# Optimization experiments

Hardware: AMD Instinct MI355X
Metric: run time of the kernel (lower is better)

The kernel has to match this reference:

```python
import jax, jax.numpy as jnp
import numpy as np

N = 50000      # nodes
E = 800000     # edges (before self-loops)
G = 128        # graphs in batch
IN = 128       # in_channels
HID = 32       # hidden_channels (per head)
HEADS = 4
OUT = 64       # out_channels
SLOPE = 0.2    # PyG GATConv default negative_slope


def setup_inputs() -> dict:
    key = jax.random.key(0)
    ks = jax.random.split(key, 24)
    s = 0.1
    inp = {
        'x': jax.random.normal(ks[0], (N, IN), jnp.float32),
        'edge_index': jax.random.randint(ks[1], (2, E), 0, N, dtype=jnp.int32),
        'batch': jnp.sort(jax.random.randint(ks[2], (N,), 0, G, dtype=jnp.int32)),
        # conv1: IN -> HEADS*HID, concat
        'W1': jax.random.normal(ks[3], (IN, HEADS * HID), jnp.float32) * s,
        'a1s': jax.random.normal(ks[4], (HEADS, HID), jnp.float32) * s,
        'a1d': jax.random.normal(ks[5], (HEADS, HID), jnp.float32) * s,
        'b1': jnp.zeros((HEADS * HID,), jnp.float32),
        # conv2: HEADS*HID -> HEADS*HID, concat
        'W2': jax.random.normal(ks[6], (HEADS * HID, HEADS * HID), jnp.float32) * s,
        'a2s': jax.random.normal(ks[7], (HEADS, HID), jnp.float32) * s,
        'a2d': jax.random.normal(ks[8], (HEADS, HID), jnp.float32) * s,
        'b2': jnp.zeros((HEADS * HID,), jnp.float32),
        # conv3
        'W3': jax.random.normal(ks[9], (HEADS * HID, HEADS * HID), jnp.float32) * s,
        'a3s': jax.random.normal(ks[10], (HEADS, HID), jnp.float32) * s,
        'a3d': jax.random.normal(ks[11], (HEADS, HID), jnp.float32) * s,
        'b3': jnp.zeros((HEADS * HID,), jnp.float32),
        # conv4: heads=1, concat=False -> HID
        'W4': jax.random.normal(ks[12], (HEADS * HID, 1 * HID), jnp.float32) * s,
        'a4s': jax.random.normal(ks[13], (1, HID), jnp.float32) * s,
        'a4d': jax.random.normal(ks[14], (1, HID), jnp.float32) * s,
        'b4': jnp.zeros((HID,), jnp.float32),
        # fc: HID -> OUT
        'fcW': jax.random.normal(ks[15], (HID, OUT), jnp.float32) * s,
        'fcb': jnp.zeros((OUT,), jnp.float32),
    }
    return inp


def gat_conv(x, src, dst, W, a_src, a_dst, bias, heads, ch, concat):
    # x: [N, F_in]; src/dst: [E'] with self-loops (PyG add_self_loops=True)
    h = (x @ W).reshape(N, heads, ch)                       # [N, H, C]
    alpha_s = jnp.einsum('nhc,hc->nh', h, a_src)            # [N, H]
    alpha_d = jnp.einsum('nhc,hc->nh', h, a_dst)
    e = jax.nn.leaky_relu(alpha_s[src] + alpha_d[dst], SLOPE)  # [E', H]
    # segment softmax over edges grouped by destination node
    e_max = jax.ops.segment_max(e, dst, num_segments=N)
    e = jnp.exp(e - e_max[dst])
    denom = jax.ops.segment_sum(e, dst, num_segments=N)
    alpha = e / (denom[dst] + 1e-16)                        # [E', H]
    msg = h[src] * alpha[:, :, None]                        # [E', H, C]
    out = jax.ops.segment_sum(msg, dst, num_segments=N)     # [N, H, C]
    out = out.reshape(N, heads * ch) if concat else out.mean(axis=1)
    return out + bias


def reference(x, edge_index, batch, W1, a1s, a1d, b1, W2, a2s, a2d, b2,
              W3, a3s, a3d, b3, W4, a4s, a4d, b4, fcW, fcb):
    loop = jnp.arange(N, dtype=edge_index.dtype)
    src = jnp.concatenate([edge_index[0], loop])            # add self-loops once
    dst = jnp.concatenate([edge_index[1], loop])
    h = jax.nn.elu(gat_conv(x, src, dst, W1, a1s, a1d, b1, HEADS, HID, True))
    h = jax.nn.elu(gat_conv(h, src, dst, W2, a2s, a2d, b2, HEADS, HID, True))
    h = jax.nn.elu(gat_conv(h, src, dst, W3, a3s, a3d, b3, HEADS, HID, True))
    h = jax.nn.elu(gat_conv(h, src, dst, W4, a4s, a4d, b4, 1, HID, False))
    # global mean pool over graphs
    counts = jax.ops.segment_sum(jnp.ones((N,), h.dtype), batch, num_segments=G)
    pooled = jax.ops.segment_sum(h, batch, num_segments=G) / jnp.maximum(counts, 1.0)[:, None]
    # dropout p=0.5 is identity at inference
    return pooled @ fcW + fcb                               # [G, OUT]
```

## Files before the change

kernel.cpp:

```cpp
#include <hip/hip_runtime.h>
#include <hip/hip_bf16.h>


constexpr int NN     = 50000;
constexpr int NNPAD  = 50048;
constexpr int EE     = 800000;
constexpr int ETOT   = EE + NN;
constexpr int GG     = 128;
constexpr int HIDC   = 32;
constexpr int OUTC   = 64;

constexpr int NRANGE = (NN + 127) / 128;
constexpr int EPB    = 4096;
constexpr int NBLK   = (EE + EPB - 1) / EPB;
constexpr int RCAP   = 2688;

typedef short  bf16x8 __attribute__((ext_vector_type(8)));
typedef float  f32x4  __attribute__((ext_vector_type(4)));

static __device__ __forceinline__ unsigned short f2bf(float f) {
    __hip_bfloat16 h = __float2bfloat16(f);
    unsigned short u; __builtin_memcpy(&u, &h, 2); return u;
}
static __device__ __forceinline__ unsigned int f2bf2(float lo, float hi) {
    __hip_bfloat162 h2 = __float22bfloat162_rn(make_float2(lo, hi));
    unsigned int u; __builtin_memcpy(&u, &h2, 4); return u;
}
static __device__ __forceinline__ float bflo(unsigned int v) {
    return __uint_as_float(v << 16);
}
static __device__ __forceinline__ float bfhi(unsigned int v) {
    return __uint_as_float(v & 0xffff0000u);
}
static __device__ __forceinline__ float elu(float v) {
    return (v > 0.f) ? v : (__expf(v) - 1.f);
}
static __device__ __forceinline__ float leaky(float e) {
    return fmaxf(e, 0.f) + 0.2f * fminf(e, 0.f);
}

static __device__ void local_sort_body(
    char* smem, const int* __restrict__ ei,
    unsigned int* __restrict__ blocksorted, int* __restrict__ boffs, int b)
{
    unsigned int* sorted = reinterpret_cast<unsigned int*>(smem);
    int* hist  = reinterpret_cast<int*>(smem + EPB * 4);
    int* scanv = hist + (NRANGE + 1);
    int* cur   = scanv + (NRANGE + 1);
    int* wsum4 = cur + (NRANGE + 1);
    int* ct_s  = wsum4 + 4;

    const int tid = threadIdx.x;
    const int lane = tid & 63, wid = tid >> 6;
    const int e0 = b * EPB;
    const int ecnt = min(EPB, EE - e0);

    for (int t = tid; t < NRANGE + 1; t += 256) hist[t] = 0;
    __syncthreads();

    unsigned int recs[16];
    int rkey[16];
#pragma unroll
    for (int k = 0; k < 16; ++k) {
        const int idx = tid + k * 256;
        rkey[k] = -1;
        if (idx < ecnt) {
            const int src = ei[e0 + idx];
            const int dst = ei[EE + e0 + idx];
            const int r = dst >> 7;
            recs[k] = (unsigned int)src | ((unsigned int)(dst & 127) << 16);
            rkey[k] = r;
            atomicAdd(&hist[r], 1);
        }
    }
    __syncthreads();

    int carry = 0;
    for (int base = 0; base < NRANGE + 1; base += 256) {
        const int i = base + tid;
        const int v = (i < NRANGE + 1) ? hist[i] : 0;
        int incl = v;
#pragma unroll
        for (int off = 1; off < 64; off <<= 1) {
            int t = __shfl_up(incl, off, 64);
            if (lane >= off) incl += t;
        }
        if (lane == 63) wsum4[wid] = incl;
        __syncthreads();
        if (tid == 0) {
            int s = 0;
#pragma unroll
            for (int w = 0; w < 4; ++w) { int t = wsum4[w]; wsum4[w] = s; s += t; }
            *ct_s = s;
        }
        __syncthreads();
        const int excl = carry + wsum4[wid] + incl - v;
        if (i < NRANGE + 1) { scanv[i] = excl; cur[i] = excl; }
        carry += *ct_s;
        __syncthreads();
    }

#pragma unroll
    for (int k = 0; k < 16; ++k) {
        if (rkey[k] >= 0) {
            const int pos = atomicAdd(&cur[rkey[k]], 1);
            sorted[pos] = recs[k];
        }
    }
    __syncthreads();

    for (int t = tid; t < ecnt; t += 256)
        blocksorted[(size_t)b * EPB + t] = sorted[t];
    for (int t = tid; t < NRANGE + 1; t += 256)
        boffs[b * (NRANGE + 1) + t] = scanv[t];
}

template<int F_OUT, int NH, bool XF32>
static __device__ void gemm_body(
    char* smem, const void* __restrict__ xv,
    const unsigned short* __restrict__ wtg,
    unsigned short* __restrict__ hb,
    float* __restrict__ as_out, float* __restrict__ ad_out, int bid)
{
    constexpr int F_STG = F_OUT + 16;
    unsigned short* wt = reinterpret_cast<unsigned short*>(smem);
    const int tid = threadIdx.x;

    {
        const bf16x8* __restrict__ wg = reinterpret_cast<const bf16x8*>(wtg);
        bf16x8* wl = reinterpret_cast<bf16x8*>(wt);
        constexpr int NV = F_STG * 16;
#pragma unroll
        for (int i = 0; i < NV / 256; ++i)
            wl[i * 256 + tid] = wg[i * 256 + tid];
    }
    __syncthreads();

    const int wave = tid >> 6, lane = tid & 63;
    const int kchunk = (lane >> 4) * 8;
    const int kb_base = (lane >> 4) * 16;

#pragma unroll
    for (int rr = 0; rr < 2; ++rr) {
        const int row0 = bid * 128 + rr * 64 + wave * 16;
        const int arow = row0 + (lane & 15);

        bf16x8 a[4];
        if (XF32) {
            if (arow < NN) {
                const float* __restrict__ ap = (const float*)xv + (size_t)arow * 128;
#pragma unroll
                for (int ks = 0; ks < 4; ++ks) {
                    const float4 f0 = *reinterpret_cast<const float4*>(ap + ks * 32 + kchunk);
                    const float4 f1 = *reinterpret_cast<const float4*>(ap + ks * 32 + kchunk + 4);
                    uint4 u;
                    u.x = f2bf2(f0.x, f0.y);
                    u.y = f2bf2(f0.z, f0.w);
                    u.z = f2bf2(f1.x, f1.y);
                    u.w = f2bf2(f1.z, f1.w);
                    bf16x8 v; __builtin_memcpy(&v, &u, 16);
                    a[ks] = v;
                }
            } else {
#pragma unroll
                for (int ks = 0; ks < 4; ++ks) a[ks] = bf16x8{0,0,0,0,0,0,0,0};
            }
        } else {
            const unsigned short* __restrict__ ap =
                (const unsigned short*)xv + (size_t)arow * 128;
#pragma unroll
            for (int ks = 0; ks < 4; ++ks)
                a[ks] = *reinterpret_cast<const bf16x8*>(ap + ks * 32 + kchunk);
        }

        const int rbase = row0 + (lane >> 4) * 4;

#pragma unroll
        for (int nt = 0; nt < F_OUT / 16; ++nt) {
            const int n = nt * 16 + (lane & 15);
            f32x4 acc = {0.f, 0.f, 0.f, 0.f};
#pragma unroll
            for (int ks = 0; ks < 4; ++ks) {
                const int byte = n * 256 + ((ks * 64 + kb_base) ^ ((n & 7) << 4));
                bf16x8 b = *reinterpret_cast<const bf16x8*>(
                    reinterpret_cast<const char*>(wt) + byte);
                acc = __builtin_amdgcn_mfma_f32_16x16x32_bf16(a[ks], b, acc, 0, 0, 0);
            }
#pragma unroll
            for (int r = 0; r < 4; ++r) {
                const int row = rbase + r;
                if (row < NN)
                    hb[(size_t)row * F_OUT + n] = f2bf(acc[r]);
            }
        }

        {
            const int n = F_OUT + (lane & 15);
            f32x4 acc = {0.f, 0.f, 0.f, 0.f};
#pragma unroll
            for (int ks = 0; ks < 4; ++ks) {
                const int byte = n * 256 + ((ks * 64 + kb_base) ^ ((n & 7) << 4));
                bf16x8 b = *reinterpret_cast<const bf16x8*>(
                    reinterpret_cast<const char*>(wt) + byte);
                acc = __builtin_amdgcn_mfma_f32_16x16x32_bf16(a[ks], b, acc, 0, 0, 0);
            }
            const int col = lane & 15;
            if (col < 8) {
                const int hh = col & 3;
                const bool is_d = col >= 4;
                if (hh < NH) {
                    float* op = is_d ? ad_out : as_out;
#pragma unroll
                    for (int r = 0; r < 4; ++r) {
                        const int row = rbase + r;
                        if (row < NN) {
                            if (NH == 4) op[row * 4 + hh] = acc[r];
                            else         op[row]          = acc[r];
                        }
                    }
                }
            }
        }
    }
}

constexpr int FUSED_SMEM = 144 * 128 * 2;

__global__ __launch_bounds__(256) void fused_ls_gemm1_kernel(
    const int* __restrict__ ei,
    unsigned int* __restrict__ blocksorted,
    int* __restrict__ boffs,
    const float* __restrict__ x,
    const unsigned short* __restrict__ wtg,
    unsigned short* __restrict__ hb,
    float* __restrict__ as_out, float* __restrict__ ad_out)
{
    __shared__ char smem[FUSED_SMEM];
    if (blockIdx.x < NBLK)
        local_sort_body(smem, ei, blocksorted, boffs, blockIdx.x);
    else
        gemm_body<128, 4, true>(smem, x, wtg, hb, as_out, ad_out,
                                blockIdx.x - NBLK);
}

template<int F_OUT, int NH>
__global__ __launch_bounds__(256) void gemm_mfma_kernel(
    const void* __restrict__ xv,
    const unsigned short* __restrict__ wtg,
    unsigned short* __restrict__ hb,
    float* __restrict__ as_out, float* __restrict__ ad_out)
{
    __shared__ char smem[(F_OUT + 16) * 128 * 2];
    gemm_body<F_OUT, NH, false>(smem, xv, wtg, hb, as_out, ad_out, blockIdx.x);
}

__global__ __launch_bounds__(256) void rtot_kernel(const int* __restrict__ boffs,
                                                   int* __restrict__ rtot)
{
    const int r = blockIdx.x * 4 + (threadIdx.x >> 6);
    const int lane = threadIdx.x & 63;
    if (r >= NRANGE) return;
    int tot = 0;
    for (int b = lane; b < NBLK; b += 64) {
        const int* bp = boffs + b * (NRANGE + 1) + r;
        tot += bp[1] - bp[0];
    }
#pragma unroll
    for (int k = 1; k < 64; k <<= 1) tot += __shfl_xor(tot, k, 64);
    if (lane == 0) rtot[r] = tot + min(128, NN - r * 128);
}

__global__ __launch_bounds__(512) void rscan_kernel(const int* __restrict__ rtot,
                                                    int* __restrict__ rbase)
{
    __shared__ int wsum[8], wpre[8];
    const int tid = threadIdx.x, lane = tid & 63, wid = tid >> 6;
    int tot = (tid < NRANGE) ? rtot[tid] : 0;
    int incl = tot;
#pragma unroll
    for (int off = 1; off < 64; off <<= 1) {
        int t = __shfl_up(incl, off, 64);
        if (lane >= off) incl += t;
    }
    if (lane == 63) wsum[wid] = incl;
    __syncthreads();
    if (tid < 8) {
        int wv = wsum[tid], winc = wv;
#pragma unroll
        for (int off = 1; off < 8; off <<= 1) {
            int t = __shfl_up(winc, off, 64);
            if (tid >= off) winc += t;
        }
        wpre[tid] = winc - wv;
    }
    __syncthreads();
    const int excl = wpre[wid] + incl - tot;
    if (tid < NRANGE) rbase[tid] = excl;
    if (tid == NRANGE - 1) rbase[NRANGE] = excl + tot;
}

__global__ __launch_bounds__(256) void phaseB_kernel(
    const int* __restrict__ boffs,
    const unsigned int* __restrict__ blocksorted,
    const int* __restrict__ rbase,
    int* __restrict__ offs,
    unsigned int* __restrict__ csrpack)
{
    __shared__ unsigned int rec[RCAP];
    __shared__ unsigned int outpk[RCAP];
    __shared__ int runoff[NBLK + 1];
    __shared__ int bstart[NBLK];
    __shared__ int hist[128], lofs[128], cur[128];
    __shared__ int wsum4[4];
    __shared__ int tot0_s;

    const int r = blockIdx.x, tid = threadIdx.x;
    const int lane = tid & 63, wid = tid >> 6;
    const int base = r * 128;
    const int rn   = min(128, NN - base);

    int cnt = 0;
    if (tid < NBLK) {
        const int* bp = boffs + tid * (NRANGE + 1) + r;
        const int s = bp[0];
        bstart[tid] = s;
        cnt = bp[1] - s;
    }
    if (tid < 128) hist[tid] = 0;
    int incl = cnt;
#pragma unroll
    for (int off = 1; off < 64; off <<= 1) {
        int t = __shfl_up(incl, off, 64);
        if (lane >= off) incl += t;
    }
    if (lane == 63) wsum4[wid] = incl;
    __syncthreads();
    if (tid == 0) {
        int s = 0;
#pragma unroll
        for (int w = 0; w < 4; ++w) { int t = wsum4[w]; wsum4[w] = s; s += t; }
    }
    __syncthreads();
    const int excl = wsum4[wid] + incl - cnt;
    if (tid <= NBLK) runoff[tid] = excl;
    __syncthreads();

    const int tot8 = runoff[NBLK];
    for (int i = tid; i < tot8; i += 256) {
        int lo = 0, hi = NBLK;
        while (lo + 1 < hi) {
            const int mid = (lo + hi) >> 1;
            if (runoff[mid] <= i) lo = mid; else hi = mid;
        }
        rec[i] = blocksorted[(size_t)lo * EPB + bstart[lo] + (i - runoff[lo])];
    }
    for (int t = tid; t < rn; t += 256)
        rec[tot8 + t] = (unsigned int)(base + t) | ((unsigned int)t << 16);
    const int total = min(tot8 + rn, RCAP);
    __syncthreads();

    for (int t = tid; t < total; t += 256) atomicAdd(&hist[rec[t] >> 16], 1);
    __syncthreads();

    if (tid < 64) {
        int v = hist[tid], incl2 = v;
#pragma unroll
        for (int off = 1; off < 64; off <<= 1) {
            int t = __shfl_up(incl2, off, 64);
            if (tid >= off) incl2 += t;
        }
        lofs[tid] = incl2 - v;
        if (tid == 63) tot0_s = incl2;
    }
    __syncthreads();
    if (tid >= 64 && tid < 128) {
        const int l = tid & 63;
        int v = hist[tid], incl2 = v;
#pragma unroll
        for (int off = 1; off < 64; off <<= 1) {
            int t = __shfl_up(incl2, off, 64);
            if (l >= off) incl2 += t;
        }
        lofs[tid] = tot0_s + incl2 - v;
    }
    __syncthreads();

    if (tid < 128) cur[tid] = lofs[tid];
    if (tid < rn) offs[base + tid] = rbase[r] + lofs[tid];
    if (r == 0 && tid == 0) offs[NN] = rbase[NRANGE];
    __syncthreads();

    for (int t = tid; t < total; t += 256) {
        const unsigned int rc = rec[t];
        const int pos = atomicAdd(&cur[rc >> 16], 1);
        outpk[pos] = (rc & 0xffffu) | ((unsigned int)(base + (rc >> 16)) << 16);
    }
    __syncthreads();
    const int rb = rbase[r];
    for (int t = tid; t < total; t += 256) csrpack[rb + t] = outpk[t];
}

__global__ __launch_bounds__(256) void prep_kernel(
    const float* __restrict__ W1, const float* __restrict__ a1s, const float* __restrict__ a1d,
    const float* __restrict__ W2, const float* __restrict__ a2s, const float* __restrict__ a2d,
    const float* __restrict__ W3, const float* __restrict__ a3s, const float* __restrict__ a3d,
    const float* __restrict__ W4, const float* __restrict__ a4s, const float* __restrict__ a4d,
    unsigned short* __restrict__ wtg)
{
    __shared__ float ahat_s[128 * 8];
    const int l = blockIdx.x, tid = threadIdx.x;
    const float *W, *as_, *ad_;
    int fo, nh;
    if (l == 0)      { W = W1; as_ = a1s; ad_ = a1d; fo = 128; nh = 4; }
    else if (l == 1) { W = W2; as_ = a2s; ad_ = a2d; fo = 128; nh = 4; }
    else if (l == 2) { W = W3; as_ = a3s; ad_ = a3d; fo = 128; nh = 4; }
    else             { W = W4; as_ = a4s; ad_ = a4d; fo = 32;  nh = 1; }
    const int F_STG = fo + 16;

    for (int item = tid; item < 128 * 8; item += 256) {
        const int k = item >> 3, j = item & 7;
        const int hh = j & 3;
        const bool is_d = j >= 4;
        float v = 0.f;
        if (hh < nh) {
            const float* av = (is_d ? ad_ : as_) + hh * 32;
            const float* wp = W + (size_t)k * fo + hh * 32;
#pragma unroll 8
            for (int c = 0; c < 32; ++c) v = fmaf(wp[c], av[c], v);
        }
        ahat_s[item] = v;
    }
    __syncthreads();

    unsigned short* outb = wtg + (size_t)l * (144 * 128);
    for (int p = tid; p < F_STG * 64; p += 256) {
        const int n  = p % F_STG;
        const int k2 = p / F_STG;
        float w0 = 0.f, w1 = 0.f;
        if (n < fo) {
            w0 = W[(size_t)(2 * k2) * fo + n];
            w1 = W[(size_t)(2 * k2 + 1) * fo + n];
        } else {
            const int j = n - fo;
            if (j < 8) {
                w0 = ahat_s[(2 * k2) * 8 + j];
                w1 = ahat_s[(2 * k2 + 1) * 8 + j];
            }
        }
        const unsigned int packed = f2bf2(w0, w1);
        const int byte = n * 256 + ((4 * k2) ^ ((n & 7) << 4));
        *reinterpret_cast<unsigned int*>(reinterpret_cast<char*>(outb) + byte) = packed;
    }
}

template<int HEADS, int F_OUT, bool OUT_BF16>
__global__ __launch_bounds__(256) void aggregate_kernel(
    const unsigned short* __restrict__ hlin,
    const float* __restrict__ as_,
    const float* __restrict__ ad_,
    const int* __restrict__ offs,
    const unsigned int* __restrict__ csrpack,
    const float* __restrict__ bias,
    void* __restrict__ out_v)
{
    __shared__ float w_all[4][64 * HEADS];
    __shared__ int   s_all[4][64];
    const int wave = threadIdx.x >> 6;
    const int lane = threadIdx.x & 63;
    const int d    = blockIdx.x * 4 + wave;
    if (d >= NN) return;
    float* __restrict__ w_lds   = w_all[wave];
    int*   __restrict__ src_lds = s_all[wave];

    const int beg = offs[d], end = offs[d + 1];

    float ad_h[HEADS];
#pragma unroll
    for (int h = 0; h < HEADS; ++h) ad_h[h] = ad_[d * HEADS + h];

    float acc[8] = {0.f, 0.f, 0.f, 0.f, 0.f, 0.f, 0.f, 0.f};
    float dsum = 0.f;
    const int q  = (F_OUT == 128) ? (lane >> 4) : (lane >> 2);
    const int cl = (F_OUT == 128) ? (lane & 15) : (lane & 3);
    const int hd = (F_OUT == 128) ? (cl >> 2) : 0;

    for (int base = beg; base < end; base += 64) {
        const int cnt = min(64, end - base);
        {
            const int p = base + lane;
            const unsigned int pk = (p < end) ? csrpack[p] : 0u;
            const int src = (int)(pk & 0xffffu);
            src_lds[lane] = src;
            if (HEADS == 4) {
                float4 w4 = make_float4(0.f, 0.f, 0.f, 0.f);
                if (p < end) {
                    const float4 s4 = *reinterpret_cast<const float4*>(
                        as_ + (size_t)src * 4);
                    w4.x = __expf(leaky(s4.x + ad_h[0]));
                    w4.y = __expf(leaky(s4.y + ad_h[1]));
                    w4.z = __expf(leaky(s4.z + ad_h[2]));
                    w4.w = __expf(leaky(s4.w + ad_h[3]));
                }
                *reinterpret_cast<float4*>(w_lds + lane * 4) = w4;
            } else {
                float w1 = 0.f;
                if (p < end) w1 = __expf(leaky(as_[src] + ad_h[0]));
                w_lds[lane] = w1;
            }
        }
        asm volatile("s_waitcnt lgkmcnt(0)" ::: "memory");

        if (F_OUT == 128) {
            const int cntR = (cnt + 3) & ~3;
#pragma unroll 2
            for (int j = 0; j < cntR; j += 4) {
                const int   slot = j + q;
                const int   srcj = src_lds[slot];
                const float w    = w_lds[slot * 4 + hd];
                const uint4 hv   = *reinterpret_cast<const uint4*>(
                    hlin + (size_t)srcj * 128 + cl * 8);
                dsum += w;
                acc[0] = fmaf(w, bflo(hv.x), acc[0]);
                acc[1] = fmaf(w, bfhi(hv.x), acc[1]);
                acc[2] = fmaf(w, bflo(hv.y), acc[2]);
                acc[3] = fmaf(w, bfhi(hv.y), acc[3]);
                acc[4] = fmaf(w, bflo(hv.z), acc[4]);
                acc[5] = fmaf(w, bfhi(hv.z), acc[5]);
                acc[6] = fmaf(w, bflo(hv.w), acc[6]);
                acc[7] = fmaf(w, bfhi(hv.w), acc[7]);
            }
        } else {
            const int cntR = (cnt + 15) & ~15;
#pragma unroll 2
            for (int j = 0; j < cntR; j += 16) {
                const int   slot = j + q;
                const int   srcj = src_lds[slot];
                const float w    = w_lds[slot];
                const uint4 hv   = *reinterpret_cast<const uint4*>(
                    hlin + (size_t)srcj * 32 + cl * 8);
                dsum += w;
                acc[0] = fmaf(w, bflo(hv.x), acc[0]);
                acc[1] = fmaf(w, bfhi(hv.x), acc[1]);
                acc[2] = fmaf(w, bflo(hv.y), acc[2]);
                acc[3] = fmaf(w, bfhi(hv.y), acc[3]);
                acc[4] = fmaf(w, bflo(hv.z), acc[4]);
                acc[5] = fmaf(w, bfhi(hv.z), acc[5]);
                acc[6] = fmaf(w, bflo(hv.w), acc[6]);
                acc[7] = fmaf(w, bfhi(hv.w), acc[7]);
            }
        }
    }

    if (F_OUT == 128) {
#pragma unroll
        for (int t = 0; t < 8; ++t) {
            acc[t] += __shfl_xor(acc[t], 16, 64);
            acc[t] += __shfl_xor(acc[t], 32, 64);
        }
        dsum += __shfl_xor(dsum, 16, 64);
        dsum += __shfl_xor(dsum, 32, 64);
        if (lane < 16) {
            const float rinv = 1.f / (dsum + 1e-16f);
            const int c0 = lane * 8;
            float v[8];
#pragma unroll
            for (int t = 0; t < 8; ++t) v[t] = elu(fmaf(acc[t], rinv, bias[c0 + t]));
            uint4 pk;
            pk.x = f2bf2(v[0], v[1]);
            pk.y = f2bf2(v[2], v[3]);
            pk.z = f2bf2(v[4], v[5]);
            pk.w = f2bf2(v[6], v[7]);
            *reinterpret_cast<uint4*>((unsigned short*)out_v + (size_t)d * 128 + c0) = pk;
        }
    } else {
#pragma unroll
        for (int t = 0; t < 8; ++t) {
            acc[t] += __shfl_xor(acc[t], 4, 64);
            acc[t] += __shfl_xor(acc[t], 8, 64);
            acc[t] += __shfl_xor(acc[t], 16, 64);
            acc[t] += __shfl_xor(acc[t], 32, 64);
        }
        dsum += __shfl_xor(dsum, 4, 64);
        dsum += __shfl_xor(dsum, 8, 64);
        dsum += __shfl_xor(dsum, 16, 64);
        dsum += __shfl_xor(dsum, 32, 64);
        if (lane < 4) {
            const float rinv = 1.f / (dsum + 1e-16f);
            const int c0 = lane * 8;
            float v[8];
#pragma unroll
            for (int t = 0; t < 8; ++t) v[t] = elu(fmaf(acc[t], rinv, bias[c0 + t]));
            float* op = (float*)out_v + (size_t)d * 32 + c0;
            *reinterpret_cast<float4*>(op)     = make_float4(v[0], v[1], v[2], v[3]);
            *reinterpret_cast<float4*>(op + 4) = make_float4(v[4], v[5], v[6], v[7]);
        }
    }
}

__global__ __launch_bounds__(256) void pool_fc_kernel(
    const float* __restrict__ h4, const int* __restrict__ batch,
    const float* __restrict__ fcW, const float* __restrict__ fcb,
    float* __restrict__ out)
{
    const int g = blockIdx.x;
    __shared__ int sb, se;
    if (threadIdx.x == 0) {
        int lo = 0, hi = NN;
        while (lo < hi) { int mid = (lo + hi) >> 1; if (batch[mid] < g) lo = mid + 1; else hi = mid; }
        sb = lo;
        lo = sb; hi = NN;
        while (lo < hi) { int mid = (lo + hi) >> 1; if (batch[mid] < g + 1) lo = mid + 1; else hi = mid; }
        se = lo;
    }
    __syncthreads();
    const int s = sb, e = se;

    const int c  = threadIdx.x & 31;
    const int rg = threadIdx.x >> 5;
    float acc = 0.f;
    for (int n = s + rg; n < e; n += 8)
        acc += h4[(size_t)n * HIDC + c];

    __shared__ float red[8][32];
    red[rg][c] = acc;
    __syncthreads();
    __shared__ float pooled_s[32];
    if (threadIdx.x < 32) {
        float v = 0.f;
#pragma unroll
        for (int r = 0; r < 8; ++r) v += red[r][threadIdx.x];
        pooled_s[threadIdx.x] = v / fmaxf((float)(e - s), 1.f);
    }
    __syncthreads();
    if (threadIdx.x < OUTC) {
        const int o = threadIdx.x;
        float a2 = fcb[o];
#pragma unroll
        for (int cc = 0; cc < HIDC; ++cc)
            a2 = fmaf(pooled_s[cc], fcW[cc * OUTC + o], a2);
        out[g * OUTC + o] = a2;
    }
}

extern "C" void kernel_launch(void* const* d_in, const int* in_sizes, int n_in,
                              void* d_out, int out_size, void* d_ws, size_t ws_size,
                              hipStream_t stream)
{
    const float* x     = (const float*)d_in[0];
    const int*   ei    = (const int*)d_in[1];
    const int*   batch = (const int*)d_in[2];
    const float* W1  = (const float*)d_in[3];
    const float* a1s = (const float*)d_in[4];
    const float* a1d = (const float*)d_in[5];
    const float* b1  = (const float*)d_in[6];
    const float* W2  = (const float*)d_in[7];
    const float* a2s = (const float*)d_in[8];
    const float* a2d = (const float*)d_in[9];
    const float* b2  = (const float*)d_in[10];
    const float* W3  = (const float*)d_in[11];
    const float* a3s = (const float*)d_in[12];
    const float* a3d = (const float*)d_in[13];
    const float* b3  = (const float*)d_in[14];
    const float* W4  = (const float*)d_in[15];
    const float* a4s = (const float*)d_in[16];
    const float* a4d = (const float*)d_in[17];
    const float* b4  = (const float*)d_in[18];
    const float* fcW = (const float*)d_in[19];
    const float* fcb = (const float*)d_in[20];
    float* out = (float*)d_out;

    unsigned short* xb = (unsigned short*)d_ws;
    unsigned short* hb = xb + (size_t)NNPAD * 128;
    float* asb  = (float*)(hb + (size_t)NNPAD * 128);
    float* adb  = asb + (size_t)NN * 4;
    int*   offs    = (int*)(adb + (size_t)NN * 4);
    unsigned int* csrpack = (unsigned int*)(offs + NN + 1);
    int*   boffs  = (int*)(csrpack + ETOT);
    int*   rbase  = boffs + NBLK * (NRANGE + 1);
    int*   rtot   = rbase + NRANGE + 1;
    unsigned short* wtg = (unsigned short*)(rtot + NRANGE);
    unsigned int* blocksorted = (unsigned int*)(wtg + 4 * 144 * 128);
    float* bufF = (float*)xb;

    prep_kernel<<<4, 256, 0, stream>>>(W1, a1s, a1d, W2, a2s, a2d,
                                       W3, a3s, a3d, W4, a4s, a4d, wtg);

    constexpr int GEMM_GRID = NNPAD / 128;
    constexpr int AGG_GRID  = (NN + 3) / 4;
    constexpr size_t WSTRIDE = 144 * 128;

    fused_ls_gemm1_kernel<<<NBLK + GEMM_GRID, 256, 0, stream>>>(
        ei, blocksorted, boffs, x, wtg + 0 * WSTRIDE, hb, asb, adb);

    rtot_kernel<<<(NRANGE + 3) / 4, 256, 0, stream>>>(boffs, rtot);
    rscan_kernel<<<1, 512, 0, stream>>>(rtot, rbase);
    phaseB_kernel<<<NRANGE, 256, 0, stream>>>(boffs, blocksorted, rbase, offs, csrpack);

    aggregate_kernel<4, 128, true><<<AGG_GRID, 256, 0, stream>>>(hb, asb, adb, offs, csrpack, b1, xb);
    gemm_mfma_kernel<128, 4><<<GEMM_GRID, 256, 0, stream>>>(xb, wtg + 1 * WSTRIDE, hb, asb, adb);
    aggregate_kernel<4, 128, true><<<AGG_GRID, 256, 0, stream>>>(hb, asb, adb, offs, csrpack, b2, xb);
    gemm_mfma_kernel<128, 4><<<GEMM_GRID, 256, 0, stream>>>(xb, wtg + 2 * WSTRIDE, hb, asb, adb);
    aggregate_kernel<4, 128, true><<<AGG_GRID, 256, 0, stream>>>(hb, asb, adb, offs, csrpack, b3, xb);
    gemm_mfma_kernel<32, 1><<<GEMM_GRID, 256, 0, stream>>>(xb, wtg + 3 * WSTRIDE, hb, asb, adb);
    aggregate_kernel<1, 32, false><<<AGG_GRID, 256, 0, stream>>>(hb, asb, adb, offs, csrpack, b4, bufF);

    pool_fc_kernel<<<GG, 256, 0, stream>>>(bufF, batch, fcW, fcb, out);
}
```

Before: 240.4 us.

## Fold rtot into local sort via atomics and batch gather loads in aggregation

```diff
diff --git a/kernel.cpp b/kernel.cpp
--- a/kernel.cpp
+++ b/kernel.cpp
@@ -41,7 +41,8 @@
 
 static __device__ void local_sort_body(
     char* smem, const int* __restrict__ ei,
-    unsigned int* __restrict__ blocksorted, int* __restrict__ boffs, int b)
+    unsigned int* __restrict__ blocksorted, int* __restrict__ boffs,
+    int* __restrict__ rtot, int b)
 {
     unsigned int* sorted = reinterpret_cast<unsigned int*>(smem);
     int* hist  = reinterpret_cast<int*>(smem + EPB * 4);
@@ -74,6 +75,11 @@
         }
     }
     __syncthreads();
+
+    for (int t = tid; t < NRANGE; t += 256) {
+        const int h = hist[t];
+        if (h) atomicAdd(&rtot[t], h);
+    }
 
     int carry = 0;
     for (int base = 0; base < NRANGE + 1; base += 256) {
@@ -230,6 +236,7 @@
     const int* __restrict__ ei,
     unsigned int* __restrict__ blocksorted,
     int* __restrict__ boffs,
+    int* __restrict__ rtot,
     const float* __restrict__ x,
     const unsigned short* __restrict__ wtg,
     unsigned short* __restrict__ hb,
@@ -237,7 +244,7 @@
 {
     __shared__ char smem[FUSED_SMEM];
     if (blockIdx.x < NBLK)
-        local_sort_body(smem, ei, blocksorted, boffs, blockIdx.x);
+        local_sort_body(smem, ei, blocksorted, boffs, rtot, blockIdx.x);
     else
         gemm_body<128, 4, true>(smem, x, wtg, hb, as_out, ad_out,
                                 blockIdx.x - NBLK);
@@ -252,22 +259,6 @@
 {
     __shared__ char smem[(F_OUT + 16) * 128 * 2];
     gemm_body<F_OUT, NH, false>(smem, xv, wtg, hb, as_out, ad_out, blockIdx.x);
-}
-
-__global__ __launch_bounds__(256) void rtot_kernel(const int* __restrict__ boffs,
-                                                   int* __restrict__ rtot)
-{
-    const int r = blockIdx.x * 4 + (threadIdx.x >> 6);
-    const int lane = threadIdx.x & 63;
-    if (r >= NRANGE) return;
-    int tot = 0;
-    for (int b = lane; b < NBLK; b += 64) {
-        const int* bp = boffs + b * (NRANGE + 1) + r;
-        tot += bp[1] - bp[0];
-    }
-#pragma unroll
-    for (int k = 1; k < 64; k <<= 1) tot += __shfl_xor(tot, k, 64);
-    if (lane == 0) rtot[r] = tot + min(128, NN - r * 128);
 }
 
 __global__ __launch_bounds__(512) void rscan_kernel(const int* __restrict__ rtot,
@@ -405,10 +396,15 @@
     const float* __restrict__ W2, const float* __restrict__ a2s, const float* __restrict__ a2d,
     const float* __restrict__ W3, const float* __restrict__ a3s, const float* __restrict__ a3d,
     const float* __restrict__ W4, const float* __restrict__ a4s, const float* __restrict__ a4d,
-    unsigned short* __restrict__ wtg)
+    unsigned short* __restrict__ wtg, int* __restrict__ rtot)
 {
     __shared__ float ahat_s[128 * 8];
     const int l = blockIdx.x, tid = threadIdx.x;
+
+    if (l == 0)
+        for (int t = tid; t < NRANGE; t += 256)
+            rtot[t] = min(128, NN - t * 128);
+
     const float *W, *as_, *ad_;
     int fo, nh;
     if (l == 0)      { W = W1; as_ = a1s; ad_ = a1d; fo = 128; nh = 4; }
@@ -480,73 +476,90 @@
 
     float acc[8] = {0.f, 0.f, 0.f, 0.f, 0.f, 0.f, 0.f, 0.f};
     float dsum = 0.f;
+    constexpr int STEP = (F_OUT == 128) ? 4 : 16;
+    constexpr int G1   = (F_OUT == 128) ? 8 : 4;
+    constexpr int SPL  = (F_OUT == 128) ? 16 : 4;
     const int q  = (F_OUT == 128) ? (lane >> 4) : (lane >> 2);
     const int cl = (F_OUT == 128) ? (lane & 15) : (lane & 3);
     const int hd = (F_OUT == 128) ? (cl >> 2) : 0;
 
     for (int base = beg; base < end; base += 64) {
         const int cnt = min(64, end - base);
-        {
-            const int p = base + lane;
-            const unsigned int pk = (p < end) ? csrpack[p] : 0u;
-            const int src = (int)(pk & 0xffffu);
-            src_lds[lane] = src;
-            if (HEADS == 4) {
-                float4 w4 = make_float4(0.f, 0.f, 0.f, 0.f);
-                if (p < end) {
-                    const float4 s4 = *reinterpret_cast<const float4*>(
-                        as_ + (size_t)src * 4);
-                    w4.x = __expf(leaky(s4.x + ad_h[0]));
-                    w4.y = __expf(leaky(s4.y + ad_h[1]));
-                    w4.z = __expf(leaky(s4.z + ad_h[2]));
-                    w4.w = __expf(leaky(s4.w + ad_h[3]));
+        const int nsl = (cnt + STEP - 1) / STEP;
+
+        const int p = base + lane;
+        const unsigned int pk = (p < end) ? csrpack[p] : 0u;
+        src_lds[lane] = (int)(pk & 0xffffu);
+        asm volatile("s_waitcnt lgkmcnt(0)" ::: "memory");
+
+        uint4 hv[G1];
+#pragma unroll
+        for (int i = 0; i < G1; ++i) {
+            if (i < nsl) {
+                const int srcj = src_lds[i * STEP + q];
+                hv[i] = *reinterpret_cast<const uint4*>(
+                    hlin + (size_t)srcj * F_OUT + cl * 8);
+            }
+        }
+
+        if (HEADS == 4) {
+            float4 w4 = make_float4(0.f, 0.f, 0.f, 0.f);
+            if (p < end) {
+                const int src = (int)(pk & 0xffffu);
+                const float4 s4 = *reinterpret_cast<const float4*>(
+                    as_ + (size_t)src * 4);
+                w4.x = __expf(leaky(s4.x + ad_h[0]));
+                w4.y = __expf(leaky(s4.y + ad_h[1]));
+                w4.z = __expf(leaky(s4.z + ad_h[2]));
+                w4.w = __expf(leaky(s4.w + ad_h[3]));
+            }
+            *reinterpret_cast<float4*>(w_lds + lane * 4) = w4;
+        } else {
+            float w1 = 0.f;
+            if (p < end) {
+                const int src = (int)(pk & 0xffffu);
+                w1 = __expf(leaky(as_[src] + ad_h[0]));
+            }
+            w_lds[lane] = w1;
+        }
+        asm volatile("s_waitcnt lgkmcnt(0)" ::: "memory");
+
+#pragma unroll
+        for (int i = 0; i < G1; ++i) {
+            if (i < nsl) {
+                const int slot = i * STEP + q;
+                const float w = (HEADS == 4) ? w_lds[slot * 4 + hd] : w_lds[slot];
+                dsum += w;
+                acc[0] = fmaf(w, bflo(hv[i].x), acc[0]);
+                acc[1] = fmaf(w, bfhi(hv[i].x), acc[1]);
+                acc[2] = fmaf(w, bflo(hv[i].y), acc[2]);
+                acc[3] = fmaf(w, bfhi(hv[i].y), acc[3]);
+                acc[4] = fmaf(w, bflo(hv[i].z), acc[4]);
+                acc[5] = fmaf(w, bfhi(hv[i].z), acc[5]);
+                acc[6] = fmaf(w, bflo(hv[i].w), acc[6]);
+                acc[7] = fmaf(w, bfhi(hv[i].w), acc[7]);
+            }
+        }
+
+        if (SPL > G1 && nsl > G1) {
+#pragma unroll
+            for (int i = G1; i < SPL; ++i) {
+                if (i < nsl) {
+                    const int slot = i * STEP + q;
+                    const int srcj = src_lds[slot];
+                    const uint4 h2 = *reinterpret_cast<const uint4*>(
+                        hlin + (size_t)srcj * F_OUT + cl * 8);
+                    const float w = (HEADS == 4) ? w_lds[slot * 4 + hd] : w_lds[slot];
+                    dsum += w;
+                    acc[0] = fmaf(w, bflo(h2.x), acc[0]);
+                    acc[1] = fmaf(w, bfhi(h2.x), acc[1]);
+                    acc[2] = fmaf(w, bflo(h2.y), acc[2]);
+                    acc[3] = fmaf(w, bfhi(h2.y), acc[3]);
+                    acc[4] = fmaf(w, bflo(h2.z), acc[4]);
+                    acc[5] = fmaf(w, bfhi(h2.z), acc[5]);
+                    acc[6] = fmaf(w, bflo(h2.w), acc[6]);
+                    acc[7] = fmaf(w, bfhi(h2.w), acc[7]);
                 }
-                *reinterpret_cast<float4*>(w_lds + lane * 4) = w4;
-            } else {
-                float w1 = 0.f;
-                if (p < end) w1 = __expf(leaky(as_[src] + ad_h[0]));
-                w_lds[lane] = w1;
-            }
-        }
-        asm volatile("s_waitcnt lgkmcnt(0)" ::: "memory");
-
-        if (F_OUT == 128) {
-            const int cntR = (cnt + 3) & ~3;
-#pragma unroll 2
-            for (int j = 0; j < cntR; j += 4) {
-                const int   slot = j + q;
-                const int   srcj = src_lds[slot];
-                const float w    = w_lds[slot * 4 + hd];
-                const uint4 hv   = *reinterpret_cast<const uint4*>(
-                    hlin + (size_t)srcj * 128 + cl * 8);
-                dsum += w;
-                acc[0] = fmaf(w, bflo(hv.x), acc[0]);
-                acc[1] = fmaf(w, bfhi(hv.x), acc[1]);
-                acc[2] = fmaf(w, bflo(hv.y), acc[2]);
-                acc[3] = fmaf(w, bfhi(hv.y), acc[3]);
-                acc[4] = fmaf(w, bflo(hv.z), acc[4]);
-                acc[5] = fmaf(w, bfhi(hv.z), acc[5]);
-                acc[6] = fmaf(w, bflo(hv.w), acc[6]);
-                acc[7] = fmaf(w, bfhi(hv.w), acc[7]);
-            }
-        } else {
-            const int cntR = (cnt + 15) & ~15;
-#pragma unroll 2
-            for (int j = 0; j < cntR; j += 16) {
-                const int   slot = j + q;
-                const int   srcj = src_lds[slot];
-                const float w    = w_lds[slot];
-                const uint4 hv   = *reinterpret_cast<const uint4*>(
-                    hlin + (size_t)srcj * 32 + cl * 8);
-                dsum += w;
-                acc[0] = fmaf(w, bflo(hv.x), acc[0]);
-                acc[1] = fmaf(w, bfhi(hv.x), acc[1]);
-                acc[2] = fmaf(w, bflo(hv.y), acc[2]);
-                acc[3] = fmaf(w, bfhi(hv.y), acc[3]);
-                acc[4] = fmaf(w, bflo(hv.z), acc[4]);
-                acc[5] = fmaf(w, bfhi(hv.z), acc[5]);
-                acc[6] = fmaf(w, bflo(hv.w), acc[6]);
-                acc[7] = fmaf(w, bfhi(hv.w), acc[7]);
             }
         }
     }
@@ -565,12 +578,12 @@
             float v[8];
 #pragma unroll
             for (int t = 0; t < 8; ++t) v[t] = elu(fmaf(acc[t], rinv, bias[c0 + t]));
-            uint4 pk;
-            pk.x = f2bf2(v[0], v[1]);
-            pk.y = f2bf2(v[2], v[3]);
-            pk.z = f2bf2(v[4], v[5]);
-            pk.w = f2bf2(v[6], v[7]);
-            *reinterpret_cast<uint4*>((unsigned short*)out_v + (size_t)d * 128 + c0) = pk;
+            uint4 pk2;
+            pk2.x = f2bf2(v[0], v[1]);
+            pk2.y = f2bf2(v[2], v[3]);
+            pk2.z = f2bf2(v[4], v[5]);
+            pk2.w = f2bf2(v[6], v[7]);
+            *reinterpret_cast<uint4*>((unsigned short*)out_v + (size_t)d * 128 + c0) = pk2;
         }
     } else {
 #pragma unroll
@@ -683,16 +696,15 @@
     float* bufF = (float*)xb;
 
     prep_kernel<<<4, 256, 0, stream>>>(W1, a1s, a1d, W2, a2s, a2d,
-                                       W3, a3s, a3d, W4, a4s, a4d, wtg);
+                                       W3, a3s, a3d, W4, a4s, a4d, wtg, rtot);
 
     constexpr int GEMM_GRID = NNPAD / 128;
     constexpr int AGG_GRID  = (NN + 3) / 4;
     constexpr size_t WSTRIDE = 144 * 128;
 
     fused_ls_gemm1_kernel<<<NBLK + GEMM_GRID, 256, 0, stream>>>(
-        ei, blocksorted, boffs, x, wtg + 0 * WSTRIDE, hb, asb, adb);
-
-    rtot_kernel<<<(NRANGE + 3) / 4, 256, 0, stream>>>(boffs, rtot);
+        ei, blocksorted, boffs, rtot, x, wtg + 0 * WSTRIDE, hb, asb, adb);
+
     rscan_kernel<<<1, 512, 0, stream>>>(rtot, rbase);
     phaseB_kernel<<<NRANGE, 256, 0, stream>>>(boffs, blocksorted, rbase, offs, csrpack);
 
```

After: 268.0 us. 1.11x slower.
